# Optimization experiments

Measured on AMD Instinct MI355X. Metric: run time of the kernel, lower is better.

The kernel has to match this reference:

```python
import jax, jax.numpy as jnp
import numpy as np

D_MODEL = 1024
NUM_HEADS = 16
D_K = D_MODEL // NUM_HEADS
D_FF = 4096
THETA = 10000.0
EPS = 1e-5


def rmsnorm(x, w):
    ms = jnp.mean(jnp.square(x), axis=-1, keepdims=True)
    return x * jax.lax.rsqrt(ms + EPS) * w


def rope(x, pos):
    # x: [B, H, S, d_k]; pos: [S]
    half = x.shape[-1] // 2
    inv_freq = THETA ** (-jnp.arange(half, dtype=x.dtype) * 2.0 / x.shape[-1])  # [half]
    ang = pos.astype(x.dtype)[:, None] * inv_freq[None, :]  # [S, half]
    cos, sin = jnp.cos(ang), jnp.sin(ang)
    xe, xo = x[..., 0::2], x[..., 1::2]
    oe = xe * cos - xo * sin
    oo = xe * sin + xo * cos
    return jnp.stack([oe, oo], axis=-1).reshape(x.shape)


def setup_inputs() -> dict:
    key = jax.random.key(0)
    ks = jax.random.split(key, 10)
    std_d = 1.0 / np.sqrt(D_MODEL)
    std_f = 1.0 / np.sqrt(D_FF)
    B, S = 4, 2048
    return {
        "x": jax.random.normal(ks[0], (B, S, D_MODEL), dtype=jnp.float32),
        "token_positions": jnp.arange(S, dtype=jnp.int32),
        "q_proj": jax.random.normal(ks[1], (D_MODEL, D_MODEL), dtype=jnp.float32) * std_d,
        "k_proj": jax.random.normal(ks[2], (D_MODEL, D_MODEL), dtype=jnp.float32) * std_d,
        "v_proj": jax.random.normal(ks[3], (D_MODEL, D_MODEL), dtype=jnp.float32) * std_d,
        "o_proj": jax.random.normal(ks[4], (D_MODEL, D_MODEL), dtype=jnp.float32) * std_d,
        "w1": jax.random.normal(ks[5], (D_FF, D_MODEL), dtype=jnp.float32) * std_d,
        "w2": jax.random.normal(ks[6], (D_MODEL, D_FF), dtype=jnp.float32) * std_f,
        "w3": jax.random.normal(ks[7], (D_FF, D_MODEL), dtype=jnp.float32) * std_d,
        "ln1_w": jnp.ones((D_MODEL,), dtype=jnp.float32),
        "ln2_w": jnp.ones((D_MODEL,), dtype=jnp.float32),
    }


def reference(x, token_positions, q_proj, k_proj, v_proj, o_proj, w1, w2, w3, ln1_w, ln2_w):
    B, S, _ = x.shape
    x_ln = rmsnorm(x, ln1_w)
    q = x_ln @ q_proj.T
    k = x_ln @ k_proj.T
    v = x_ln @ v_proj.T
    # [B, S, D] -> [B, H, S, d_k]
    def split_heads(t):
        return t.reshape(B, S, NUM_HEADS, D_K).transpose(0, 2, 1, 3)
    q, k, v = split_heads(q), split_heads(k), split_heads(v)
    q = rope(q, token_positions)
    k = rope(k, token_positions)
    scores = jnp.einsum("bhqd,bhkd->bhqk", q, k) / jnp.sqrt(jnp.asarray(D_K, x.dtype))
    causal = jnp.tril(jnp.ones((S, S), dtype=bool))
    scores = jnp.where(causal, scores, -jnp.inf)
    attn = jax.nn.softmax(scores, axis=-1)
    out = jnp.einsum("bhqk,bhkd->bhqd", attn, v)
    out = out.transpose(0, 2, 1, 3).reshape(B, S, D_MODEL)
    x = x + out @ o_proj.T
    x_ln2 = rmsnorm(x, ln2_w)
    u = x_ln2 @ w1.T
    vff = x_ln2 @ w3.T
    ff = (u * jax.nn.sigmoid(u)) * vff
    return x + ff @ w2.T
```

## Files before the change

kernel.cpp:

```cpp
#include <hip/hip_runtime.h>
#include <hip/hip_bf16.h>


typedef unsigned short u16;
typedef __attribute__((ext_vector_type(8))) short short8;
typedef __attribute__((ext_vector_type(4))) float f32x4;
typedef __attribute__((ext_vector_type(16))) float f32x16;

#define MFMA16(a, b, c) __builtin_amdgcn_mfma_f32_16x16x32_bf16(a, b, c, 0, 0, 0)
#define MFMA32(a, b, c) __builtin_amdgcn_mfma_f32_32x32x16_bf16(a, b, c, 0, 0, 0)

__device__ __forceinline__ u16 f2b(float f) {
  union { float f; unsigned u; } x; x.f = f;
  unsigned r = x.u + 0x7FFFu + ((x.u >> 16) & 1u);
  return (u16)(r >> 16);
}
__device__ __forceinline__ float b2f(u16 h) {
  union { unsigned u; float f; } x; x.u = ((unsigned)h) << 16;
  return x.f;
}
__device__ __forceinline__ unsigned pkbf(float a, float b) {
  __hip_bfloat162 h = __float22bfloat162_rn(make_float2(a, b));
  union { __hip_bfloat162 h; unsigned u; } cv; cv.h = h;
  return cv.u;
}
__device__ __forceinline__ void async16(const void* g, void* l) {
  __builtin_amdgcn_global_load_lds(
      (const __attribute__((address_space(1))) void*)g,
      (__attribute__((address_space(3))) void*)l, 16, 0, 0);
}

template <int MODE>
__global__ __launch_bounds__(256, 2) void gemm_bt(
    const u16* __restrict__ A, const u16* __restrict__ B,
    u16* __restrict__ Cb, float* __restrict__ Cf, const float* __restrict__ R,
    int M, int N, int K) {
  __shared__ __align__(16) u16 As[128 * 64];
  __shared__ __align__(16) u16 Bs[128 * 64];
  const int tid = threadIdx.x;
  const int l = tid & 63, w = tid >> 6;
  const int wr = w & 1, wc = w >> 1;
  const int lr = l & 31, lh = l >> 5;
  const size_t m0 = (size_t)blockIdx.y * 128, n0 = (size_t)blockIdx.x * 128;
  f32x16 acc[2][2] = {};
  for (int k0 = 0; k0 < K; k0 += 64) {
#pragma unroll
    for (int t = 0; t < 4; ++t) {
      int c = t * 256 + tid;
      int r = c >> 3;
      int gc = ((c & 7) ^ (r & 7)) << 3;
      async16(A + (m0 + r) * (size_t)K + k0 + gc, &As[c * 8]);
    }
#pragma unroll
    for (int t = 0; t < 4; ++t) {
      int c = t * 256 + tid;
      int r = c >> 3;
      int gc = ((c & 7) ^ (r & 7)) << 3;
      async16(B + (n0 + r) * (size_t)K + k0 + gc, &Bs[c * 8]);
    }
    __syncthreads();
#pragma unroll
    for (int c = 0; c < 4; ++c) {
      const int c8 = c * 2 + lh;
      short8 af[2], bfr[2];
#pragma unroll
      for (int mi = 0; mi < 2; ++mi) {
        int r = wr * 64 + mi * 32 + lr;
        af[mi] = *(const short8*)&As[r * 64 + ((c8 ^ (r & 7)) << 3)];
      }
#pragma unroll
      for (int ni = 0; ni < 2; ++ni) {
        int r = wc * 64 + ni * 32 + lr;
        bfr[ni] = *(const short8*)&Bs[r * 64 + ((c8 ^ (r & 7)) << 3)];
      }
#pragma unroll
      for (int mi = 0; mi < 2; ++mi)
#pragma unroll
        for (int ni = 0; ni < 2; ++ni)
          acc[mi][ni] = MFMA32(af[mi], bfr[ni], acc[mi][ni]);
    }
    __syncthreads();
  }
#pragma unroll
  for (int mi = 0; mi < 2; ++mi)
#pragma unroll
    for (int ni = 0; ni < 2; ++ni) {
      size_t n = n0 + wc * 64 + ni * 32 + lr;
#pragma unroll
      for (int reg = 0; reg < 16; ++reg) {
        size_t m = m0 + wr * 64 + mi * 32 + (reg & 3) + 8 * (reg >> 2) + 4 * lh;
        float v = acc[mi][ni][reg];
        if (MODE == 0)
          Cb[m * (size_t)N + n] = f2b(v);
        else
          Cf[m * (size_t)N + n] = v + R[m * (size_t)N + n];
      }
    }
}

__global__ __launch_bounds__(256, 2) void ffn_gemm(
    const u16* __restrict__ A, const u16* __restrict__ B1,
    const u16* __restrict__ B3, u16* __restrict__ Hout, int M, int N, int K) {
  __shared__ __align__(16) u16 As[128 * 64];
  __shared__ __align__(16) u16 B1s[128 * 64];
  __shared__ __align__(16) u16 B3s[128 * 64];
  const int tid = threadIdx.x;
  const int l = tid & 63, w = tid >> 6;
  const int wr = w & 1, wc = w >> 1;
  const int lr = l & 31, lh = l >> 5;
  const size_t m0 = (size_t)blockIdx.y * 128, n0 = (size_t)blockIdx.x * 128;
  f32x16 a1[2][2] = {}, a3[2][2] = {};
  for (int k0 = 0; k0 < K; k0 += 64) {
#pragma unroll
    for (int t = 0; t < 4; ++t) {
      int c = t * 256 + tid;
      int r = c >> 3;
      int gc = ((c & 7) ^ (r & 7)) << 3;
      async16(A + (m0 + r) * (size_t)K + k0 + gc, &As[c * 8]);
      async16(B1 + (n0 + r) * (size_t)K + k0 + gc, &B1s[c * 8]);
      async16(B3 + (n0 + r) * (size_t)K + k0 + gc, &B3s[c * 8]);
    }
    __syncthreads();
#pragma unroll
    for (int c = 0; c < 4; ++c) {
      const int c8 = c * 2 + lh;
      short8 af[2], b1f[2], b3f[2];
#pragma unroll
      for (int mi = 0; mi < 2; ++mi) {
        int r = wr * 64 + mi * 32 + lr;
        af[mi] = *(const short8*)&As[r * 64 + ((c8 ^ (r & 7)) << 3)];
      }
#pragma unroll
      for (int ni = 0; ni < 2; ++ni) {
        int r = wc * 64 + ni * 32 + lr;
        b1f[ni] = *(const short8*)&B1s[r * 64 + ((c8 ^ (r & 7)) << 3)];
        b3f[ni] = *(const short8*)&B3s[r * 64 + ((c8 ^ (r & 7)) << 3)];
      }
#pragma unroll
      for (int mi = 0; mi < 2; ++mi)
#pragma unroll
        for (int ni = 0; ni < 2; ++ni) {
          a1[mi][ni] = MFMA32(af[mi], b1f[ni], a1[mi][ni]);
          a3[mi][ni] = MFMA32(af[mi], b3f[ni], a3[mi][ni]);
        }
    }
    __syncthreads();
  }
#pragma unroll
  for (int mi = 0; mi < 2; ++mi)
#pragma unroll
    for (int ni = 0; ni < 2; ++ni) {
      size_t n = n0 + wc * 64 + ni * 32 + lr;
#pragma unroll
      for (int reg = 0; reg < 16; ++reg) {
        size_t m = m0 + wr * 64 + mi * 32 + (reg & 3) + 8 * (reg >> 2) + 4 * lh;
        float u = a1[mi][ni][reg];
        float g = u / (1.0f + __expf(-u));
        Hout[m * (size_t)N + n] = f2b(g * a3[mi][ni][reg]);
      }
    }
}

__global__ __launch_bounds__(256, 2) void attn_k(
    const u16* __restrict__ qh, const u16* __restrict__ kh,
    const u16* __restrict__ vt, u16* __restrict__ aout) {
  __shared__ __align__(16) u16 Ks[128 * 64];
  __shared__ __align__(16) u16 Vs[64 * 128];
  __shared__ __align__(16) u16 Ps[128 * 136];
  const int tid = threadIdx.x;
  const int l = tid & 63, w = tid >> 6;
  const int q = l & 15, lq = l >> 4;
  const int q0 = (int)(gridDim.x - 1 - blockIdx.x) * 128;
  const int bh = blockIdx.y;
  const size_t base = (size_t)bh * (2048 * 64);
  const int nt = (q0 >> 7) + 1;

  int qcol[2] = {q0 + w * 16 + q, q0 + 64 + w * 16 + q};
  short8 bq[2][2];
#pragma unroll
  for (int sub = 0; sub < 2; ++sub)
#pragma unroll
    for (int kk = 0; kk < 2; ++kk)
      bq[sub][kk] = *(const short8*)(qh + base + (size_t)qcol[sub] * 64 + kk * 32 + lq * 8);

  f32x4 o[2][4] = {};
  float mI[2] = {-1e30f, -1e30f}, lI[2] = {0.0f, 0.0f};
  u16* pr0 = &Ps[(w * 16 + q) * 136];
  u16* pr1 = &Ps[(64 + w * 16 + q) * 136];

  for (int it = 0; it < nt; ++it) {
    const int kv0 = it << 7;
    if (it) __syncthreads();
#pragma unroll
    for (int t = 0; t < 4; ++t) {
      int p = t * 256 + tid;
      int r = p >> 3, cs = p & 7;
      async16(kh + base + (size_t)(kv0 + r) * 64 + ((cs ^ (r & 7)) << 3), &Ks[p * 8]);
    }
#pragma unroll
    for (int t = 0; t < 4; ++t) {
      int p = t * 256 + tid;
      int r = p >> 4, cs = p & 15;
      async16(vt + base + (size_t)r * 2048 + kv0 + ((cs ^ (r & 15)) << 3), &Vs[p * 8]);
    }
    __syncthreads();
    const bool last = (it == nt - 1);

    f32x4 s[2][8] = {};
#pragma unroll
    for (int kk = 0; kk < 2; ++kk) {
#pragma unroll
      for (int mt = 0; mt < 8; ++mt) {
        int row = mt * 16 + q;
        short8 ak = *(const short8*)&Ks[row * 64 + (((kk * 4 + lq) ^ (q & 7)) << 3)];
        s[0][mt] = MFMA16(ak, bq[0][kk], s[0][mt]);
        s[1][mt] = MFMA16(ak, bq[1][kk], s[1][mt]);
      }
    }
    if (last) {
#pragma unroll
      for (int sub = 0; sub < 2; ++sub)
#pragma unroll
        for (int mt = 0; mt < 8; ++mt)
#pragma unroll
          for (int r = 0; r < 4; ++r)
            if (kv0 + mt * 16 + lq * 4 + r > qcol[sub]) s[sub][mt][r] = -1e30f;
    }
#pragma unroll
    for (int sub = 0; sub < 2; ++sub) {
      float mx = -1e30f;
#pragma unroll
      for (int mt = 0; mt < 8; ++mt)
#pragma unroll
        for (int r = 0; r < 4; ++r) mx = fmaxf(mx, s[sub][mt][r]);
      mx = fmaxf(mx, __shfl_xor(mx, 16, 64));
      mx = fmaxf(mx, __shfl_xor(mx, 32, 64));
      const float mn = fmaxf(mI[sub], mx);
      const float al = exp2f(mI[sub] - mn);
      mI[sub] = mn;
      float rs = 0.0f;
#pragma unroll
      for (int mt = 0; mt < 8; ++mt)
#pragma unroll
        for (int r = 0; r < 4; ++r) {
          float p = exp2f(s[sub][mt][r] - mn);
          s[sub][mt][r] = p;
          rs += p;
        }
      rs += __shfl_xor(rs, 16, 64);
      rs += __shfl_xor(rs, 32, 64);
      lI[sub] = lI[sub] * al + rs;
#pragma unroll
      for (int mt = 0; mt < 4; ++mt)
#pragma unroll
        for (int r = 0; r < 4; ++r) o[sub][mt][r] *= al;
      u16* pr = sub ? pr1 : pr0;
#pragma unroll
      for (int mt = 0; mt < 8; ++mt) {
        uint2 pd;
        pd.x = pkbf(s[sub][mt][0], s[sub][mt][1]);
        pd.y = pkbf(s[sub][mt][2], s[sub][mt][3]);
        *(uint2*)&pr[mt * 16 + lq * 4] = pd;
      }
    }
#pragma unroll
    for (int kk = 0; kk < 4; ++kk) {
      short8 bp0 = *(const short8*)&pr0[kk * 32 + lq * 8];
      short8 bp1 = *(const short8*)&pr1[kk * 32 + lq * 8];
#pragma unroll
      for (int mt = 0; mt < 4; ++mt) {
        int row = mt * 16 + q;
        short8 av = *(const short8*)&Vs[row * 128 + (((kk * 4 + lq) ^ (row & 15)) << 3)];
        o[0][mt] = MFMA16(av, bp0, o[0][mt]);
        o[1][mt] = MFMA16(av, bp1, o[1][mt]);
      }
    }
  }
  const int b = bh >> 4, h = bh & 15;
#pragma unroll
  for (int sub = 0; sub < 2; ++sub) {
    const float inv = 1.0f / lI[sub];
#pragma unroll
    for (int mt = 0; mt < 4; ++mt) {
      uint2 pd;
      pd.x = pkbf(o[sub][mt][0] * inv, o[sub][mt][1] * inv);
      pd.y = pkbf(o[sub][mt][2] * inv, o[sub][mt][3] * inv);
      *(uint2*)&aout[((size_t)(b * 2048 + qcol[sub])) * 1024 + h * 64 + mt * 16 + lq * 4] = pd;
    }
  }
}

__global__ __launch_bounds__(256) void rmsnorm_k(
    const float* __restrict__ x, const float* __restrict__ w, u16* __restrict__ out) {
  const int row = blockIdx.x;
  const int tid = threadIdx.x;
  const float4 v = ((const float4*)(x + (size_t)row * 1024))[tid];
  float ss = v.x * v.x + v.y * v.y + v.z * v.z + v.w * v.w;
#pragma unroll
  for (int d = 1; d < 64; d <<= 1) ss += __shfl_xor(ss, d, 64);
  __shared__ float red[4];
  if ((tid & 63) == 0) red[tid >> 6] = ss;
  __syncthreads();
  const float sc = rsqrtf((red[0] + red[1] + red[2] + red[3]) * (1.0f / 1024.0f) + 1e-5f);
  const float4 wv = ((const float4*)w)[tid];
  u16* o = out + (size_t)row * 1024 + tid * 4;
  o[0] = f2b(v.x * sc * wv.x);
  o[1] = f2b(v.y * sc * wv.y);
  o[2] = f2b(v.z * sc * wv.z);
  o[3] = f2b(v.w * sc * wv.w);
}

__global__ __launch_bounds__(256) void rope_k(
    const u16* __restrict__ qkv, u16* __restrict__ qh, u16* __restrict__ kh,
    const int* __restrict__ pos) {
  int idx = blockIdx.x * 256 + threadIdx.x;
  int grp = idx & 255;
  int row = idx >> 8;
  int which = grp >> 7;
  int p = grp & 127;
  int s = row & 2047, b = row >> 11;
  int h = p >> 3, gi = p & 7;
  const u16* src = qkv + (size_t)row * 3072 + which * 1024 + h * 64 + gi * 8;
  uint4 in = *(const uint4*)src;
  const u16* e = (const u16*)&in;
  const float fp = (float)pos[s];
  const float scale = which ? 1.0f : 0.18033688011112042f;
  uint4 outv;
  unsigned* ov = (unsigned*)&outv;
#pragma unroll
  for (int j = 0; j < 4; ++j) {
    int i = gi * 4 + j;
    float xe = b2f(e[2 * j]), xo = b2f(e[2 * j + 1]);
    float inv = exp2f(-(float)(2 * i) * (13.287712379549449f / 64.0f));
    float ang = fp * inv;
    float sn, cs;
    __sincosf(ang, &sn, &cs);
    ov[j] = pkbf((xe * cs - xo * sn) * scale, (xe * sn + xo * cs) * scale);
  }
  u16* dst = (which ? kh : qh) + (((size_t)(b * 16 + h)) * 2048 + s) * 64 + gi * 8;
  *(uint4*)dst = outv;
}

__global__ __launch_bounds__(256) void transv_k(
    const u16* __restrict__ qkv, u16* __restrict__ vt) {
  __shared__ u16 t[64][65];
  const int bh = blockIdx.y, s0 = blockIdx.x * 64;
  const int b = bh >> 4, h = bh & 15;
  const int tid = threadIdx.x;
#pragma unroll
  for (int i = 0; i < 16; ++i) {
    int e = i * 256 + tid;
    int sl = e >> 6, d = e & 63;
    t[sl][d] = qkv[((size_t)(b * 2048 + s0 + sl)) * 3072 + 2048 + h * 64 + d];
  }
  __syncthreads();
#pragma unroll
  for (int i = 0; i < 16; ++i) {
    int e = i * 256 + tid;
    int d = e >> 6, sl = e & 63;
    vt[((size_t)(bh * 64 + d)) * 2048 + s0 + sl] = t[sl][d];
  }
}

__global__ __launch_bounds__(256) void cvt_all(
    const float* __restrict__ qp, const float* __restrict__ kp,
    const float* __restrict__ vp, const float* __restrict__ op,
    const float* __restrict__ w1, const float* __restrict__ w3,
    const float* __restrict__ w2,
    u16* __restrict__ WQKV, u16* __restrict__ WO,
    u16* __restrict__ W1, u16* __restrict__ W3, u16* __restrict__ W2) {
  int i = blockIdx.x * 256 + threadIdx.x;
  const float* src;
  u16* dst;
  int off;
  if (i < 1048576) {
    int seg = i >> 18, within = i & 262143;
    src = (seg == 0) ? qp : (seg == 1) ? kp : (seg == 2) ? vp : op;
    dst = (seg == 3) ? WO : WQKV + (size_t)seg * 1048576;
    off = within;
  } else {
    int j = i - 1048576;
    int seg = j >> 20;
    off = j & 1048575;
    src = (seg == 0) ? w1 : (seg == 1) ? w3 : w2;
    dst = (seg == 0) ? W1 : (seg == 1) ? W3 : W2;
  }
  float4 v = ((const float4*)src)[off];
  u16* o = dst + (size_t)off * 4;
  o[0] = f2b(v.x); o[1] = f2b(v.y); o[2] = f2b(v.z); o[3] = f2b(v.w);
}

extern "C" void kernel_launch(void* const* d_in, const int* in_sizes, int n_in,
                              void* d_out, int out_size, void* d_ws, size_t ws_size,
                              hipStream_t stream) {
  const float* x   = (const float*)d_in[0];
  const int*   pos = (const int*)d_in[1];
  const float* qp  = (const float*)d_in[2];
  const float* kp  = (const float*)d_in[3];
  const float* vp  = (const float*)d_in[4];
  const float* op  = (const float*)d_in[5];
  const float* w1  = (const float*)d_in[6];
  const float* w2  = (const float*)d_in[7];
  const float* w3  = (const float*)d_in[8];
  const float* ln1 = (const float*)d_in[9];
  const float* ln2 = (const float*)d_in[10];
  float* out = (float*)d_out;
  char* ws = (char*)d_ws;
  const size_t MB = 1024 * 1024;

  u16* WQKV = (u16*)(ws + 0 * MB);
  u16* WO   = (u16*)(ws + 6 * MB);
  u16* W1   = (u16*)(ws + 8 * MB);
  u16* W3   = (u16*)(ws + 16 * MB);
  u16* W2   = (u16*)(ws + 24 * MB);
  u16* XLN  = (u16*)(ws + 32 * MB);
  u16* QKV  = (u16*)(ws + 48 * MB);
  u16* QH   = (u16*)(ws + 96 * MB);
  u16* KH   = (u16*)(ws + 112 * MB);
  u16* VT   = (u16*)(ws + 128 * MB);
  u16* ATT  = (u16*)(ws + 48 * MB);
  u16* XLN2 = (u16*)(ws + 64 * MB);
  u16* Hbuf = (u16*)(ws + 80 * MB);
  (void)in_sizes; (void)n_in; (void)out_size; (void)ws_size;

  cvt_all<<<16384, 256, 0, stream>>>(qp, kp, vp, op, w1, w3, w2,
                                     WQKV, WO, W1, W3, W2);
  rmsnorm_k<<<8192, 256, 0, stream>>>(x, ln1, XLN);
  gemm_bt<0><<<dim3(24, 64), 256, 0, stream>>>(XLN, WQKV, QKV, nullptr, nullptr, 8192, 3072, 1024);
  rope_k<<<8192, 256, 0, stream>>>(QKV, QH, KH, pos);
  transv_k<<<dim3(32, 64), 256, 0, stream>>>(QKV, VT);
  attn_k<<<dim3(16, 64), 256, 0, stream>>>(QH, KH, VT, ATT);
  gemm_bt<1><<<dim3(8, 64), 256, 0, stream>>>(ATT, WO, nullptr, out, x, 8192, 1024, 1024);
  rmsnorm_k<<<8192, 256, 0, stream>>>(out, ln2, XLN2);
  ffn_gemm<<<dim3(32, 64), 256, 0, stream>>>(XLN2, W1, W3, Hbuf, 8192, 4096, 1024);
  gemm_bt<1><<<dim3(8, 64), 256, 0, stream>>>(Hbuf, W2, nullptr, out, out, 8192, 1024, 4096);
}
```

Before: 637.6 us.

## Use 256x256 double-buffered GEMM tiles and split fused FFN gate GEMM

Replaces the 128x128 single-buffered GEMM with a 512-thread, 256x256-tile kernel. It double-buffers LDS tiles so the next K slice loads while MFMAs run, and raises wave priority around the MFMAs. The fused W1/W3 FFN kernel becomes two passes: the first writes SiLU(u) as bf16 and the second reads it back and multiplies by v. The split adds an extra bf16 round trip of the hidden activation and rounds the gate to bf16 before the product. The larger tiles also mean fewer blocks per GEMM (128 for the output projections), which may underfill the GPU.

```diff
diff --git a/kernel.cpp b/kernel.cpp
--- a/kernel.cpp
+++ b/kernel.cpp
@@ -31,132 +31,90 @@
 }
 
 template <int MODE>
-__global__ __launch_bounds__(256, 2) void gemm_bt(
+__global__ __launch_bounds__(512, 1) void gemm5(
     const u16* __restrict__ A, const u16* __restrict__ B,
     u16* __restrict__ Cb, float* __restrict__ Cf, const float* __restrict__ R,
     int M, int N, int K) {
-  __shared__ __align__(16) u16 As[128 * 64];
-  __shared__ __align__(16) u16 Bs[128 * 64];
+  __shared__ __align__(16) u16 As[2][256 * 64];
+  __shared__ __align__(16) u16 Bs[2][256 * 64];
   const int tid = threadIdx.x;
   const int l = tid & 63, w = tid >> 6;
-  const int wr = w & 1, wc = w >> 1;
+  const int wm = w >> 2, wn = w & 3;
   const int lr = l & 31, lh = l >> 5;
-  const size_t m0 = (size_t)blockIdx.y * 128, n0 = (size_t)blockIdx.x * 128;
-  f32x16 acc[2][2] = {};
-  for (int k0 = 0; k0 < K; k0 += 64) {
-#pragma unroll
-    for (int t = 0; t < 4; ++t) {
-      int c = t * 256 + tid;
-      int r = c >> 3;
-      int gc = ((c & 7) ^ (r & 7)) << 3;
-      async16(A + (m0 + r) * (size_t)K + k0 + gc, &As[c * 8]);
-    }
-#pragma unroll
-    for (int t = 0; t < 4; ++t) {
-      int c = t * 256 + tid;
-      int r = c >> 3;
-      int gc = ((c & 7) ^ (r & 7)) << 3;
-      async16(B + (n0 + r) * (size_t)K + k0 + gc, &Bs[c * 8]);
-    }
-    __syncthreads();
+  const size_t m0 = (size_t)blockIdx.y * 256, n0 = (size_t)blockIdx.x * 256;
+  f32x16 acc[4][2] = {};
+
+#define STAGE_TILE(buf, kt)                                                  \
+  {                                                                          \
+    const size_t kofs = (size_t)(kt) * 64;                                   \
+    _Pragma("unroll") for (int tt = 0; tt < 4; ++tt) {                       \
+      int p = tt * 512 + tid;                                                \
+      int r = p >> 3;                                                        \
+      int gc = ((p & 7) ^ (r & 7)) << 3;                                     \
+      async16(A + (m0 + r) * (size_t)K + kofs + gc, &As[buf][p * 8]);        \
+      async16(B + (n0 + r) * (size_t)K + kofs + gc, &Bs[buf][p * 8]);        \
+    }                                                                        \
+  }
+
+  const int NT = K >> 6;
+  STAGE_TILE(0, 0);
+  for (int t = 0; t < NT; ++t) {
+    const int cur = t & 1;
+    if (t + 1 < NT) {
+      STAGE_TILE(cur ^ 1, t + 1);
+      asm volatile("s_waitcnt vmcnt(8)" ::: "memory");
+    } else {
+      asm volatile("s_waitcnt vmcnt(0)" ::: "memory");
+    }
+    __builtin_amdgcn_sched_barrier(0);
+    __builtin_amdgcn_s_barrier();
 #pragma unroll
     for (int c = 0; c < 4; ++c) {
       const int c8 = c * 2 + lh;
-      short8 af[2], bfr[2];
-#pragma unroll
-      for (int mi = 0; mi < 2; ++mi) {
-        int r = wr * 64 + mi * 32 + lr;
-        af[mi] = *(const short8*)&As[r * 64 + ((c8 ^ (r & 7)) << 3)];
+      short8 af[4], bf2[2];
+#pragma unroll
+      for (int mi = 0; mi < 4; ++mi) {
+        int r = wm * 128 + mi * 32 + lr;
+        af[mi] = *(const short8*)&As[cur][r * 64 + ((c8 ^ (r & 7)) << 3)];
       }
 #pragma unroll
       for (int ni = 0; ni < 2; ++ni) {
-        int r = wc * 64 + ni * 32 + lr;
-        bfr[ni] = *(const short8*)&Bs[r * 64 + ((c8 ^ (r & 7)) << 3)];
-      }
-#pragma unroll
-      for (int mi = 0; mi < 2; ++mi)
+        int r = wn * 64 + ni * 32 + lr;
+        bf2[ni] = *(const short8*)&Bs[cur][r * 64 + ((c8 ^ (r & 7)) << 3)];
+      }
+      __builtin_amdgcn_s_setprio(1);
+#pragma unroll
+      for (int mi = 0; mi < 4; ++mi)
 #pragma unroll
         for (int ni = 0; ni < 2; ++ni)
-          acc[mi][ni] = MFMA32(af[mi], bfr[ni], acc[mi][ni]);
-    }
-    __syncthreads();
-  }
-#pragma unroll
-  for (int mi = 0; mi < 2; ++mi)
+          acc[mi][ni] = MFMA32(af[mi], bf2[ni], acc[mi][ni]);
+      __builtin_amdgcn_s_setprio(0);
+    }
+    asm volatile("s_waitcnt lgkmcnt(0)" ::: "memory");
+    __builtin_amdgcn_sched_barrier(0);
+    __builtin_amdgcn_s_barrier();
+  }
+#undef STAGE_TILE
+
+#pragma unroll
+  for (int mi = 0; mi < 4; ++mi)
 #pragma unroll
     for (int ni = 0; ni < 2; ++ni) {
-      size_t n = n0 + wc * 64 + ni * 32 + lr;
+      size_t n = n0 + wn * 64 + ni * 32 + lr;
 #pragma unroll
       for (int reg = 0; reg < 16; ++reg) {
-        size_t m = m0 + wr * 64 + mi * 32 + (reg & 3) + 8 * (reg >> 2) + 4 * lh;
+        size_t m = m0 + wm * 128 + mi * 32 + (reg & 3) + 8 * (reg >> 2) + 4 * lh;
         float v = acc[mi][ni][reg];
-        if (MODE == 0)
+        if (MODE == 0) {
           Cb[m * (size_t)N + n] = f2b(v);
-        else
+        } else if (MODE == 1) {
           Cf[m * (size_t)N + n] = v + R[m * (size_t)N + n];
-      }
-    }
-}
-
-__global__ __launch_bounds__(256, 2) void ffn_gemm(
-    const u16* __restrict__ A, const u16* __restrict__ B1,
-    const u16* __restrict__ B3, u16* __restrict__ Hout, int M, int N, int K) {
-  __shared__ __align__(16) u16 As[128 * 64];
-  __shared__ __align__(16) u16 B1s[128 * 64];
-  __shared__ __align__(16) u16 B3s[128 * 64];
-  const int tid = threadIdx.x;
-  const int l = tid & 63, w = tid >> 6;
-  const int wr = w & 1, wc = w >> 1;
-  const int lr = l & 31, lh = l >> 5;
-  const size_t m0 = (size_t)blockIdx.y * 128, n0 = (size_t)blockIdx.x * 128;
-  f32x16 a1[2][2] = {}, a3[2][2] = {};
-  for (int k0 = 0; k0 < K; k0 += 64) {
-#pragma unroll
-    for (int t = 0; t < 4; ++t) {
-      int c = t * 256 + tid;
-      int r = c >> 3;
-      int gc = ((c & 7) ^ (r & 7)) << 3;
-      async16(A + (m0 + r) * (size_t)K + k0 + gc, &As[c * 8]);
-      async16(B1 + (n0 + r) * (size_t)K + k0 + gc, &B1s[c * 8]);
-      async16(B3 + (n0 + r) * (size_t)K + k0 + gc, &B3s[c * 8]);
-    }
-    __syncthreads();
-#pragma unroll
-    for (int c = 0; c < 4; ++c) {
-      const int c8 = c * 2 + lh;
-      short8 af[2], b1f[2], b3f[2];
-#pragma unroll
-      for (int mi = 0; mi < 2; ++mi) {
-        int r = wr * 64 + mi * 32 + lr;
-        af[mi] = *(const short8*)&As[r * 64 + ((c8 ^ (r & 7)) << 3)];
-      }
-#pragma unroll
-      for (int ni = 0; ni < 2; ++ni) {
-        int r = wc * 64 + ni * 32 + lr;
-        b1f[ni] = *(const short8*)&B1s[r * 64 + ((c8 ^ (r & 7)) << 3)];
-        b3f[ni] = *(const short8*)&B3s[r * 64 + ((c8 ^ (r & 7)) << 3)];
-      }
-#pragma unroll
-      for (int mi = 0; mi < 2; ++mi)
-#pragma unroll
-        for (int ni = 0; ni < 2; ++ni) {
-          a1[mi][ni] = MFMA32(af[mi], b1f[ni], a1[mi][ni]);
-          a3[mi][ni] = MFMA32(af[mi], b3f[ni], a3[mi][ni]);
+        } else if (MODE == 2) {
+          Cb[m * (size_t)N + n] = f2b(v / (1.0f + __expf(-v)));
+        } else {
+          float g = b2f(Cb[m * (size_t)N + n]);
+          Cb[m * (size_t)N + n] = f2b(v * g);
         }
-    }
-    __syncthreads();
-  }
-#pragma unroll
-  for (int mi = 0; mi < 2; ++mi)
-#pragma unroll
-    for (int ni = 0; ni < 2; ++ni) {
-      size_t n = n0 + wc * 64 + ni * 32 + lr;
-#pragma unroll
-      for (int reg = 0; reg < 16; ++reg) {
-        size_t m = m0 + wr * 64 + mi * 32 + (reg & 3) + 8 * (reg >> 2) + 4 * lh;
-        float u = a1[mi][ni][reg];
-        float g = u / (1.0f + __expf(-u));
-        Hout[m * (size_t)N + n] = f2b(g * a3[mi][ni][reg]);
       }
     }
 }
@@ -419,19 +377,20 @@
   u16* KH   = (u16*)(ws + 112 * MB);
   u16* VT   = (u16*)(ws + 128 * MB);
   u16* ATT  = (u16*)(ws + 48 * MB);
-  u16* XLN2 = (u16*)(ws + 64 * MB);
-  u16* Hbuf = (u16*)(ws + 80 * MB);
+  u16* XLN2 = (u16*)(ws + 32 * MB);
+  u16* GH   = (u16*)(ws + 48 * MB);
   (void)in_sizes; (void)n_in; (void)out_size; (void)ws_size;
 
   cvt_all<<<16384, 256, 0, stream>>>(qp, kp, vp, op, w1, w3, w2,
                                      WQKV, WO, W1, W3, W2);
   rmsnorm_k<<<8192, 256, 0, stream>>>(x, ln1, XLN);
-  gemm_bt<0><<<dim3(24, 64), 256, 0, stream>>>(XLN, WQKV, QKV, nullptr, nullptr, 8192, 3072, 1024);
+  gemm5<0><<<dim3(12, 32), 512, 0, stream>>>(XLN, WQKV, QKV, nullptr, nullptr, 8192, 3072, 1024);
   rope_k<<<8192, 256, 0, stream>>>(QKV, QH, KH, pos);
   transv_k<<<dim3(32, 64), 256, 0, stream>>>(QKV, VT);
   attn_k<<<dim3(16, 64), 256, 0, stream>>>(QH, KH, VT, ATT);
-  gemm_bt<1><<<dim3(8, 64), 256, 0, stream>>>(ATT, WO, nullptr, out, x, 8192, 1024, 1024);
+  gemm5<1><<<dim3(4, 32), 512, 0, stream>>>(ATT, WO, nullptr, out, x, 8192, 1024, 1024);
   rmsnorm_k<<<8192, 256, 0, stream>>>(out, ln2, XLN2);
-  ffn_gemm<<<dim3(32, 64), 256, 0, stream>>>(XLN2, W1, W3, Hbuf, 8192, 4096, 1024);
-  gemm_bt<1><<<dim3(8, 64), 256, 0, stream>>>(Hbuf, W2, nullptr, out, out, 8192, 1024, 4096);
-}
+  gemm5<2><<<dim3(16, 32), 512, 0, stream>>>(XLN2, W1, GH, nullptr, nullptr, 8192, 4096, 1024);
+  gemm5<3><<<dim3(16, 32), 512, 0, stream>>>(XLN2, W3, GH, nullptr, nullptr, 8192, 4096, 1024);
+  gemm5<1><<<dim3(4, 32), 512, 0, stream>>>(GH, W2, nullptr, out, out, 8192, 1024, 4096);
+}
```

Measured after the change: 756.2 us. 18.6% more time.

## Pair causal query tiles per block and overlap K/V staging with compute

Applied to the files above, without the earlier changes.

The attention kernel now has each block process two query tiles (qt and 15-qt), so every block does the same amount of causal work, and the grid is halved. Within each tile loop, the next K tile is prefetched while softmax runs, and V is loaded while QK^T computes. This uses explicit vmcnt waits and raw s_barrier calls in place of __syncthreads. The goal is to remove tail imbalance from triangular causal work and to hide global-load latency, at the cost of fragile manual wait-count synchronisation.

```diff
diff --git a/kernel.cpp b/kernel.cpp
--- a/kernel.cpp
+++ b/kernel.cpp
@@ -9,6 +9,7 @@
 
 #define MFMA16(a, b, c) __builtin_amdgcn_mfma_f32_16x16x32_bf16(a, b, c, 0, 0, 0)
 #define MFMA32(a, b, c) __builtin_amdgcn_mfma_f32_32x32x16_bf16(a, b, c, 0, 0, 0)
+#define VMC(N) asm volatile("s_waitcnt vmcnt(" #N ")" ::: "memory")
 
 __device__ __forceinline__ u16 f2b(float f) {
   union { float f; unsigned u; } x; x.f = f;
@@ -170,124 +171,147 @@
   const int tid = threadIdx.x;
   const int l = tid & 63, w = tid >> 6;
   const int q = l & 15, lq = l >> 4;
-  const int q0 = (int)(gridDim.x - 1 - blockIdx.x) * 128;
   const int bh = blockIdx.y;
   const size_t base = (size_t)bh * (2048 * 64);
-  const int nt = (q0 >> 7) + 1;
-
-  int qcol[2] = {q0 + w * 16 + q, q0 + 64 + w * 16 + q};
-  short8 bq[2][2];
-#pragma unroll
-  for (int sub = 0; sub < 2; ++sub)
-#pragma unroll
-    for (int kk = 0; kk < 2; ++kk)
-      bq[sub][kk] = *(const short8*)(qh + base + (size_t)qcol[sub] * 64 + kk * 32 + lq * 8);
-
-  f32x4 o[2][4] = {};
-  float mI[2] = {-1e30f, -1e30f}, lI[2] = {0.0f, 0.0f};
-  u16* pr0 = &Ps[(w * 16 + q) * 136];
-  u16* pr1 = &Ps[(64 + w * 16 + q) * 136];
-
-  for (int it = 0; it < nt; ++it) {
-    const int kv0 = it << 7;
-    if (it) __syncthreads();
-#pragma unroll
-    for (int t = 0; t < 4; ++t) {
-      int p = t * 256 + tid;
-      int r = p >> 3, cs = p & 7;
-      async16(kh + base + (size_t)(kv0 + r) * 64 + ((cs ^ (r & 7)) << 3), &Ks[p * 8]);
-    }
-#pragma unroll
-    for (int t = 0; t < 4; ++t) {
-      int p = t * 256 + tid;
-      int r = p >> 4, cs = p & 15;
-      async16(vt + base + (size_t)r * 2048 + kv0 + ((cs ^ (r & 15)) << 3), &Vs[p * 8]);
-    }
-    __syncthreads();
-    const bool last = (it == nt - 1);
-
-    f32x4 s[2][8] = {};
-#pragma unroll
-    for (int kk = 0; kk < 2; ++kk) {
-#pragma unroll
-      for (int mt = 0; mt < 8; ++mt) {
-        int row = mt * 16 + q;
-        short8 ak = *(const short8*)&Ks[row * 64 + (((kk * 4 + lq) ^ (q & 7)) << 3)];
-        s[0][mt] = MFMA16(ak, bq[0][kk], s[0][mt]);
-        s[1][mt] = MFMA16(ak, bq[1][kk], s[1][mt]);
-      }
-    }
-    if (last) {
-#pragma unroll
-      for (int sub = 0; sub < 2; ++sub)
+  const int b = bh >> 4, h = bh & 15;
+
+#define STAGE_K(kvt)                                                          \
+  { _Pragma("unroll") for (int t = 0; t < 4; ++t) {                           \
+      int p = t * 256 + tid;                                                  \
+      int r = p >> 3, cs = p & 7;                                             \
+      async16(kh + base + (size_t)((kvt) * 128 + r) * 64 + ((cs ^ (r & 7)) << 3), \
+              &Ks[p * 8]); } }
+#define STAGE_V(kvt)                                                          \
+  { _Pragma("unroll") for (int t = 0; t < 4; ++t) {                           \
+      int p = t * 256 + tid;                                                  \
+      int r = p >> 4, cs = p & 15;                                            \
+      async16(vt + base + (size_t)r * 2048 + (kvt) * 128 + ((cs ^ (r & 15)) << 3), \
+              &Vs[p * 8]); } }
+#define BARRIER                                                               \
+  __builtin_amdgcn_sched_barrier(0);                                          \
+  __builtin_amdgcn_s_barrier();                                               \
+  __builtin_amdgcn_sched_barrier(0)
+
+#pragma unroll 1
+  for (int pass = 0; pass < 2; ++pass) {
+    const int qt = pass ? (int)blockIdx.x : 15 - (int)blockIdx.x;
+    const int q0 = qt << 7;
+    const int nt = qt + 1;
+    const int qcol[2] = {q0 + w * 16 + q, q0 + 64 + w * 16 + q};
+    short8 bq[2][2];
+#pragma unroll
+    for (int sub = 0; sub < 2; ++sub)
+#pragma unroll
+      for (int kk = 0; kk < 2; ++kk)
+        bq[sub][kk] = *(const short8*)(qh + base + (size_t)qcol[sub] * 64 + kk * 32 + lq * 8);
+
+    f32x4 o[2][4] = {};
+    float mI[2] = {-1e30f, -1e30f}, lI[2] = {0.0f, 0.0f};
+    u16* pr0 = &Ps[(w * 16 + q) * 136];
+    u16* pr1 = &Ps[(64 + w * 16 + q) * 136];
+
+    BARRIER;
+    STAGE_K(0);
+    STAGE_V(0);
+
+#pragma unroll 1
+    for (int it = 0; it < nt; ++it) {
+      if (it == 0) { VMC(4); } else { VMC(0); }
+      BARRIER;
+      if (it) STAGE_V(it);
+
+      f32x4 s[2][8] = {};
+#pragma unroll
+      for (int kk = 0; kk < 2; ++kk) {
+#pragma unroll
+        for (int mt = 0; mt < 8; ++mt) {
+          int row = mt * 16 + q;
+          short8 ak = *(const short8*)&Ks[row * 64 + (((kk * 4 + lq) ^ (q & 7)) << 3)];
+          s[0][mt] = MFMA16(ak, bq[0][kk], s[0][mt]);
+          s[1][mt] = MFMA16(ak, bq[1][kk], s[1][mt]);
+        }
+      }
+      BARRIER;
+      if (it + 1 < nt) STAGE_K(it + 1);
+
+      const bool last = (it == nt - 1);
+      if (last) {
+        const int kv0 = it << 7;
+#pragma unroll
+        for (int sub = 0; sub < 2; ++sub)
+#pragma unroll
+          for (int mt = 0; mt < 8; ++mt)
+#pragma unroll
+            for (int r = 0; r < 4; ++r)
+              if (kv0 + mt * 16 + lq * 4 + r > qcol[sub]) s[sub][mt][r] = -1e30f;
+      }
+#pragma unroll
+      for (int sub = 0; sub < 2; ++sub) {
+        float mx = -1e30f;
 #pragma unroll
         for (int mt = 0; mt < 8; ++mt)
 #pragma unroll
-          for (int r = 0; r < 4; ++r)
-            if (kv0 + mt * 16 + lq * 4 + r > qcol[sub]) s[sub][mt][r] = -1e30f;
+          for (int r = 0; r < 4; ++r) mx = fmaxf(mx, s[sub][mt][r]);
+        mx = fmaxf(mx, __shfl_xor(mx, 16, 64));
+        mx = fmaxf(mx, __shfl_xor(mx, 32, 64));
+        const float mn = fmaxf(mI[sub], mx);
+        const float al = exp2f(mI[sub] - mn);
+        mI[sub] = mn;
+        float rs = 0.0f;
+#pragma unroll
+        for (int mt = 0; mt < 8; ++mt)
+#pragma unroll
+          for (int r = 0; r < 4; ++r) {
+            float p = exp2f(s[sub][mt][r] - mn);
+            s[sub][mt][r] = p;
+            rs += p;
+          }
+        rs += __shfl_xor(rs, 16, 64);
+        rs += __shfl_xor(rs, 32, 64);
+        lI[sub] = lI[sub] * al + rs;
+#pragma unroll
+        for (int mt = 0; mt < 4; ++mt)
+#pragma unroll
+          for (int r = 0; r < 4; ++r) o[sub][mt][r] *= al;
+        u16* pr = sub ? pr1 : pr0;
+#pragma unroll
+        for (int mt = 0; mt < 8; ++mt) {
+          uint2 pd;
+          pd.x = pkbf(s[sub][mt][0], s[sub][mt][1]);
+          pd.y = pkbf(s[sub][mt][2], s[sub][mt][3]);
+          *(uint2*)&pr[mt * 16 + lq * 4] = pd;
+        }
+      }
+      if (it + 1 < nt) { VMC(4); } else { VMC(0); }
+      BARRIER;
+#pragma unroll
+      for (int kk = 0; kk < 4; ++kk) {
+        short8 bp0 = *(const short8*)&pr0[kk * 32 + lq * 8];
+        short8 bp1 = *(const short8*)&pr1[kk * 32 + lq * 8];
+#pragma unroll
+        for (int mt = 0; mt < 4; ++mt) {
+          int row = mt * 16 + q;
+          short8 av = *(const short8*)&Vs[row * 128 + (((kk * 4 + lq) ^ (row & 15)) << 3)];
+          o[0][mt] = MFMA16(av, bp0, o[0][mt]);
+          o[1][mt] = MFMA16(av, bp1, o[1][mt]);
+        }
+      }
     }
 #pragma unroll
     for (int sub = 0; sub < 2; ++sub) {
-      float mx = -1e30f;
-#pragma unroll
-      for (int mt = 0; mt < 8; ++mt)
-#pragma unroll
-        for (int r = 0; r < 4; ++r) mx = fmaxf(mx, s[sub][mt][r]);
-      mx = fmaxf(mx, __shfl_xor(mx, 16, 64));
-      mx = fmaxf(mx, __shfl_xor(mx, 32, 64));
-      const float mn = fmaxf(mI[sub], mx);
-      const float al = exp2f(mI[sub] - mn);
-      mI[sub] = mn;
-      float rs = 0.0f;
-#pragma unroll
-      for (int mt = 0; mt < 8; ++mt)
-#pragma unroll
-        for (int r = 0; r < 4; ++r) {
-          float p = exp2f(s[sub][mt][r] - mn);
-          s[sub][mt][r] = p;
-          rs += p;
-        }
-      rs += __shfl_xor(rs, 16, 64);
-      rs += __shfl_xor(rs, 32, 64);
-      lI[sub] = lI[sub] * al + rs;
-#pragma unroll
-      for (int mt = 0; mt < 4; ++mt)
-#pragma unroll
-        for (int r = 0; r < 4; ++r) o[sub][mt][r] *= al;
-      u16* pr = sub ? pr1 : pr0;
-#pragma unroll
-      for (int mt = 0; mt < 8; ++mt) {
+      const float inv = 1.0f / lI[sub];
+#pragma unroll
+      for (int mt = 0; mt < 4; ++mt) {
         uint2 pd;
-        pd.x = pkbf(s[sub][mt][0], s[sub][mt][1]);
-        pd.y = pkbf(s[sub][mt][2], s[sub][mt][3]);
-        *(uint2*)&pr[mt * 16 + lq * 4] = pd;
-      }
-    }
-#pragma unroll
-    for (int kk = 0; kk < 4; ++kk) {
-      short8 bp0 = *(const short8*)&pr0[kk * 32 + lq * 8];
-      short8 bp1 = *(const short8*)&pr1[kk * 32 + lq * 8];
-#pragma unroll
-      for (int mt = 0; mt < 4; ++mt) {
-        int row = mt * 16 + q;
-        short8 av = *(const short8*)&Vs[row * 128 + (((kk * 4 + lq) ^ (row & 15)) << 3)];
-        o[0][mt] = MFMA16(av, bp0, o[0][mt]);
-        o[1][mt] = MFMA16(av, bp1, o[1][mt]);
-      }
-    }
-  }
-  const int b = bh >> 4, h = bh & 15;
-#pragma unroll
-  for (int sub = 0; sub < 2; ++sub) {
-    const float inv = 1.0f / lI[sub];
-#pragma unroll
-    for (int mt = 0; mt < 4; ++mt) {
-      uint2 pd;
-      pd.x = pkbf(o[sub][mt][0] * inv, o[sub][mt][1] * inv);
-      pd.y = pkbf(o[sub][mt][2] * inv, o[sub][mt][3] * inv);
-      *(uint2*)&aout[((size_t)(b * 2048 + qcol[sub])) * 1024 + h * 64 + mt * 16 + lq * 4] = pd;
-    }
-  }
+        pd.x = pkbf(o[sub][mt][0] * inv, o[sub][mt][1] * inv);
+        pd.y = pkbf(o[sub][mt][2] * inv, o[sub][mt][3] * inv);
+        *(uint2*)&aout[((size_t)(b * 2048 + qcol[sub])) * 1024 + h * 64 + mt * 16 + lq * 4] = pd;
+      }
+    }
+  }
+#undef STAGE_K
+#undef STAGE_V
+#undef BARRIER
 }
 
 __global__ __launch_bounds__(256) void rmsnorm_k(
@@ -429,7 +453,7 @@
   gemm_bt<0><<<dim3(24, 64), 256, 0, stream>>>(XLN, WQKV, QKV, nullptr, nullptr, 8192, 3072, 1024);
   rope_k<<<8192, 256, 0, stream>>>(QKV, QH, KH, pos);
   transv_k<<<dim3(32, 64), 256, 0, stream>>>(QKV, VT);
-  attn_k<<<dim3(16, 64), 256, 0, stream>>>(QH, KH, VT, ATT);
+  attn_k<<<dim3(8, 64), 256, 0, stream>>>(QH, KH, VT, ATT);
   gemm_bt<1><<<dim3(8, 64), 256, 0, stream>>>(ATT, WO, nullptr, out, x, 8192, 1024, 1024);
   rmsnorm_k<<<8192, 256, 0, stream>>>(out, ln2, XLN2);
   ffn_gemm<<<dim3(32, 64), 256, 0, stream>>>(XLN2, W1, W3, Hbuf, 8192, 4096, 1024);
```

New measurement: 576.2 us. -9.6%, faster.
